# Kernel tuning notes

Hardware: AMD Instinct MI355X
Metric: run time of the kernel (lower is better)

The kernel has to match this reference:

```python
import jax, jax.numpy as jnp
import numpy as np

R = 256   # resolution
C = 16    # n_chan
F = 8     # n_freq
N = 262144


def setup_inputs() -> dict:
    key = jax.random.key(0)
    k1, k2 = jax.random.split(key)
    coords = jax.random.uniform(k1, (N, 3), dtype=jnp.float32, minval=-1.0, maxval=1.0)
    grid = jax.random.normal(k2, (3, C * F, R, R), dtype=jnp.float32) * 0.1
    # matches torch init: linspace(0,1,C*F).reshape(-1,C).T.reshape(-1)
    freqs = jnp.linspace(0.0, 1.0, C * F, dtype=jnp.float32).reshape(-1, C).T.reshape(-1)
    return {"coords": coords, "grid": grid, "freqs": freqs}


def _reflect(x, size):
    # PyTorch grid_sample reflection padding, align_corners=True:
    # reflect unnormalized coords about [0, size-1], period 2*(size-1)
    span = size - 1
    m = 2 * span
    r = jnp.abs(x) % m
    return jnp.where(r > span, m - r, r)


def _grid_sample_plane(img, xy):
    # img: (CF, R, R); xy: (Npts, 2) normalized [-1,1], (x indexes W, y indexes H)
    ix = _reflect((xy[:, 0] + 1.0) * 0.5 * (R - 1), R)
    iy = _reflect((xy[:, 1] + 1.0) * 0.5 * (R - 1), R)
    x0f = jnp.floor(ix); y0f = jnp.floor(iy)
    wx = ix - x0f; wy = iy - y0f
    x0 = jnp.clip(x0f.astype(jnp.int32), 0, R - 1)
    x1 = jnp.clip(x0 + 1, 0, R - 1)
    y0 = jnp.clip(y0f.astype(jnp.int32), 0, R - 1)
    y1 = jnp.clip(y0 + 1, 0, R - 1)
    v00 = img[:, y0, x0]  # (CF, Npts)
    v01 = img[:, y0, x1]
    v10 = img[:, y1, x0]
    v11 = img[:, y1, x1]
    return (v00 * (1 - wx) * (1 - wy) + v01 * wx * (1 - wy)
            + v10 * (1 - wx) * wy + v11 * wx * wy)


def reference(coords, grid, freqs):
    n = coords.shape[0]
    # tri-plane sample coords: plane0 (y,z), plane1 (x,z), plane2 (x,y)
    xy = jnp.stack([coords[:, (1, 2)], coords[:, (0, 2)], coords[:, (0, 1)]], 0)  # (3,N,2)
    coefs = jax.vmap(_grid_sample_plane)(grid, xy)          # (3, CF, N)
    coefs = coefs.transpose(2, 1, 0).reshape(n, C, F, 3)    # (N, C, F, 3)
    # get_freqs(): 2**(clamp(freqs,0,1)*log2(R)) - 1
    fr = 2.0 ** (jnp.clip(freqs, 0.0, 1.0) * np.float32(np.log2(R))) - 1.0  # (CF,)
    pts = (coords + 1.0) * 0.5 * (R - 1)                    # (N, 3)
    phase = (jnp.pi / R) * (pts[:, None, None, :] + 0.5) * (fr.reshape(C, F)[None, :, :, None] + 0.5)
    basis = jnp.cos(phase)                                   # (N, C, F, 3)
    # einsum BCFT,BCFT->BCT then sum over T == sum over (F, T)
    return 2.0 * jnp.sum(coefs * basis, axis=(2, 3))         # (N, C)
```

## Files before the change

### kernel.cpp

```cpp
#include <hip/hip_runtime.h>

#define RES   256
#define NCH   128
#define NC    16
#define QG    32
#define NPK   64
#define NBINS 4096

__device__ __forceinline__ unsigned int f32_to_bf16_rne(float f) {
    unsigned int u = __float_as_uint(f);
    return (u + 0x7FFFu + ((u >> 16) & 1u)) >> 16;
}
__device__ __forceinline__ float bf16_lo(unsigned int w) {
    return __uint_as_float(w << 16);
}
__device__ __forceinline__ float bf16_hi(unsigned int w) {
    return __uint_as_float(w & 0xFFFF0000u);
}
__device__ __forceinline__ float reflectf(float v) {
    float r = fabsf(v);
    r = fmodf(r, 510.0f);
    return (r > 255.0f) ? (510.0f - r) : r;
}
__device__ __forceinline__ unsigned spread3(unsigned v) {
    return (v & 1u) | ((v & 2u) << 2) | ((v & 4u) << 4) | ((v & 8u) << 6);
}
__device__ __forceinline__ int point_cell(const float* __restrict__ coords, int i) {
    const float r0 = reflectf((coords[3 * (size_t)i + 0] + 1.0f) * 127.5f);
    const float r1 = reflectf((coords[3 * (size_t)i + 1] + 1.0f) * 127.5f);
    const float r2 = reflectf((coords[3 * (size_t)i + 2] + 1.0f) * 127.5f);
    const unsigned cx = (unsigned)min(max((int)r0, 0), 255) >> 4;
    const unsigned cy = (unsigned)min(max((int)r1, 0), 255) >> 4;
    const unsigned cz = (unsigned)min(max((int)r2, 0), 255) >> 4;
    return (int)(spread3(cx) | (spread3(cy) << 1) | (spread3(cz) << 2));
}

__global__ __launch_bounds__(256) void fg_transpose_bf16(
    const float* __restrict__ in, unsigned int* __restrict__ out)
{
    __shared__ float tile[QG][RES + 4];
    const int tid = threadIdx.x;
    const int qg = blockIdx.x;
    const int y  = blockIdx.y;
    const int p  = blockIdx.z;
    const int q0 = qg * QG;

    const float* src = in + (((size_t)p * NCH + q0) * RES + y) * RES;
    #pragma unroll
    for (int it = 0; it < (QG * RES / 4) / 256; ++it) {
        const int lin = it * 256 + tid;
        const int qq = lin >> 6;
        const int x4 = lin & 63;
        *(float4*)&tile[qq][x4 * 4] =
            *(const float4*)(src + (size_t)qq * (RES * RES) + x4 * 4);
    }
    __syncthreads();
    unsigned int* dst = out + (((size_t)p * RES + y) * RES) * NPK + (q0 >> 1);
    #pragma unroll
    for (int it = 0; it < (RES * (QG / 2)) / 256; ++it) {
        const int lin = it * 256 + tid;
        const int qp = lin & 15;
        const int x  = lin >> 4;
        const unsigned int lo = f32_to_bf16_rne(tile[2 * qp + 0][x]);
        const unsigned int hi = f32_to_bf16_rne(tile[2 * qp + 1][x]);
        dst[(size_t)x * NPK + qp] = lo | (hi << 16);
    }
}

__global__ __launch_bounds__(256) void fg_hist(
    const float* __restrict__ coords, unsigned* __restrict__ hist, int n)
{
    const int i = blockIdx.x * 256 + threadIdx.x;
    if (i >= n) return;
    atomicAdd(&hist[point_cell(coords, i)], 1u);
}

__global__ __launch_bounds__(256) void fg_scan(
    const unsigned* __restrict__ hist, unsigned* __restrict__ cursor,
    const float* __restrict__ freqs, float* __restrict__ frp)
{
    __shared__ unsigned s[256];
    const int t = threadIdx.x;
    unsigned loc[16];
    unsigned sum = 0;
    #pragma unroll
    for (int k = 0; k < 16; ++k) { loc[k] = hist[t * 16 + k]; sum += loc[k]; }
    s[t] = sum;
    __syncthreads();
    for (int off = 1; off < 256; off <<= 1) {
        unsigned v = (t >= off) ? s[t - off] : 0u;
        __syncthreads();
        s[t] += v;
        __syncthreads();
    }
    unsigned base = (t == 0) ? 0u : s[t - 1];
    #pragma unroll
    for (int k = 0; k < 16; ++k) { cursor[t * 16 + k] = base; base += loc[k]; }
    if (t < 128) {
        const float f = fminf(fmaxf(freqs[t], 0.0f), 1.0f);
        frp[t] = __builtin_amdgcn_exp2f(f * 8.0f) - 0.5f;
    }
}

__global__ __launch_bounds__(256) void fg_scatter(
    const float* __restrict__ coords, unsigned* __restrict__ cursor,
    unsigned* __restrict__ perm, int n)
{
    const int i = blockIdx.x * 256 + threadIdx.x;
    if (i >= n) return;
    const unsigned pos = atomicAdd(&cursor[point_cell(coords, i)], 1u);
    perm[pos] = (unsigned)i;
}

__global__ __launch_bounds__(256) void fg_main_bf16(
    const float* __restrict__ coords,
    const unsigned int* __restrict__ grid,
    const float* __restrict__ frp_in,
    const unsigned* __restrict__ perm,
    float* __restrict__ out, int n)
{
    const int t = threadIdx.x;
    const int c = t & 15;
    const int slot = blockIdx.x * 16 + (t >> 4);
    if (slot >= n) return;
    const int i = (int)perm[slot];

    float frp[8];
    *(float4*)(frp + 0) = *(const float4*)(frp_in + c * 8 + 0);
    *(float4*)(frp + 4) = *(const float4*)(frp_in + c * 8 + 4);

    const float c0 = coords[3 * (size_t)i + 0];
    const float c1 = coords[3 * (size_t)i + 1];
    const float c2 = coords[3 * (size_t)i + 2];
    const float pts0 = (c0 + 1.0f) * 127.5f;
    const float pts1 = (c1 + 1.0f) * 127.5f;
    const float pts2 = (c2 + 1.0f) * 127.5f;

    float acc = 0.0f;

    #pragma unroll
    for (int p = 0; p < 3; ++p) {
        const float sx = (p == 0) ? pts1 : pts0;
        const float sy = (p == 2) ? pts1 : pts2;
        const float pp = (p == 0) ? pts0 : ((p == 1) ? pts1 : pts2);

        const float ix = reflectf(sx);
        const float iy = reflectf(sy);
        const float x0f = floorf(ix), y0f = floorf(iy);
        const float wx = ix - x0f, wy = iy - y0f;
        int x0 = (int)x0f; x0 = min(max(x0, 0), RES - 1);
        int y0 = (int)y0f; y0 = min(max(y0, 0), RES - 1);
        const int x1 = min(x0 + 1, RES - 1);
        const int y1 = min(y0 + 1, RES - 1);
        const float w00 = (1.0f - wx) * (1.0f - wy);
        const float w01 = wx * (1.0f - wy);
        const float w10 = (1.0f - wx) * wy;
        const float w11 = wx * wy;
        const float A = (pp + 0.5f) * (1.0f / 512.0f);

        const size_t rowbase = ((size_t)p * RES) * RES;
        const unsigned int* b00 = grid + (rowbase + (size_t)y0 * RES + x0) * NPK + c * 4;
        const unsigned int* b01 = grid + (rowbase + (size_t)y0 * RES + x1) * NPK + c * 4;
        const unsigned int* b10 = grid + (rowbase + (size_t)y1 * RES + x0) * NPK + c * 4;
        const unsigned int* b11 = grid + (rowbase + (size_t)y1 * RES + x1) * NPK + c * 4;
        const uint4 g00 = *(const uint4*)b00;
        const uint4 g01 = *(const uint4*)b01;
        const uint4 g10 = *(const uint4*)b10;
        const uint4 g11 = *(const uint4*)b11;
        const unsigned int w0[4] = {g00.x, g00.y, g00.z, g00.w};
        const unsigned int w1[4] = {g01.x, g01.y, g01.z, g01.w};
        const unsigned int w2[4] = {g10.x, g10.y, g10.z, g10.w};
        const unsigned int w3[4] = {g11.x, g11.y, g11.z, g11.w};

        #pragma unroll
        for (int jj = 0; jj < 4; ++jj) {
            const float clo = w00 * bf16_lo(w0[jj]) + w01 * bf16_lo(w1[jj])
                            + w10 * bf16_lo(w2[jj]) + w11 * bf16_lo(w3[jj]);
            const float chi = w00 * bf16_hi(w0[jj]) + w01 * bf16_hi(w1[jj])
                            + w10 * bf16_hi(w2[jj]) + w11 * bf16_hi(w3[jj]);
            const float rl = __builtin_amdgcn_fractf(A * frp[2 * jj + 0]);
            const float rh = __builtin_amdgcn_fractf(A * frp[2 * jj + 1]);
            acc += clo * __builtin_amdgcn_cosf(rl);
            acc += chi * __builtin_amdgcn_cosf(rh);
        }
    }

    out[(size_t)i * NC + c] = 2.0f * acc;
}

__global__ __launch_bounds__(256) void fg_main_f32(
    const float* __restrict__ coords,
    const float* __restrict__ grid,
    const float* __restrict__ freqs,
    float* __restrict__ out, int n)
{
    const int t = threadIdx.x;
    const int c = t & 15;
    const int i = blockIdx.x * 16 + (t >> 4);
    if (i >= n) return;

    float frp[8];
    #pragma unroll
    for (int j = 0; j < 8; ++j) {
        float f = fminf(fmaxf(freqs[c * 8 + j], 0.0f), 1.0f);
        frp[j] = __builtin_amdgcn_exp2f(f * 8.0f) - 0.5f;
    }
    const float c0 = coords[3 * (size_t)i + 0];
    const float c1 = coords[3 * (size_t)i + 1];
    const float c2 = coords[3 * (size_t)i + 2];
    const float pts0 = (c0 + 1.0f) * 127.5f;
    const float pts1 = (c1 + 1.0f) * 127.5f;
    const float pts2 = (c2 + 1.0f) * 127.5f;
    float acc = 0.0f;
    #pragma unroll
    for (int p = 0; p < 3; ++p) {
        const float sx = (p == 0) ? pts1 : pts0;
        const float sy = (p == 2) ? pts1 : pts2;
        const float pp = (p == 0) ? pts0 : ((p == 1) ? pts1 : pts2);
        const float ix = reflectf(sx);
        const float iy = reflectf(sy);
        const float x0f = floorf(ix), y0f = floorf(iy);
        const float wx = ix - x0f, wy = iy - y0f;
        int x0 = (int)x0f; x0 = min(max(x0, 0), RES - 1);
        int y0 = (int)y0f; y0 = min(max(y0, 0), RES - 1);
        const int x1 = min(x0 + 1, RES - 1);
        const int y1 = min(y0 + 1, RES - 1);
        const float w00 = (1.0f - wx) * (1.0f - wy);
        const float w01 = wx * (1.0f - wy);
        const float w10 = (1.0f - wx) * wy;
        const float w11 = wx * wy;
        const float A = (pp + 0.5f) * (1.0f / 512.0f);
        const size_t plane = (size_t)p * NCH * RES * RES;
        const int o00 = y0 * RES + x0, o01 = y0 * RES + x1;
        const int o10 = y1 * RES + x0, o11 = y1 * RES + x1;
        #pragma unroll
        for (int j = 0; j < 8; ++j) {
            const float* gq = grid + plane + (size_t)(c * 8 + j) * (RES * RES);
            const float coef = w00 * gq[o00] + w01 * gq[o01]
                             + w10 * gq[o10] + w11 * gq[o11];
            const float rr = __builtin_amdgcn_fractf(A * frp[j]);
            acc += coef * __builtin_amdgcn_cosf(rr);
        }
    }
    out[(size_t)i * NC + c] = 2.0f * acc;
}

extern "C" void kernel_launch(void* const* d_in, const int* in_sizes, int n_in,
                              void* d_out, int out_size, void* d_ws, size_t ws_size,
                              hipStream_t stream)
{
    const float* coords = (const float*)d_in[0];
    const float* grid   = (const float*)d_in[1];
    const float* freqs  = (const float*)d_in[2];
    float* out = (float*)d_out;
    const int n = in_sizes[0] / 3;

    const size_t gridT_b  = (size_t)3 * RES * RES * NPK * sizeof(unsigned);
    const size_t hist_b   = (size_t)NBINS * sizeof(unsigned);
    const size_t frp_b    = 128 * sizeof(float);
    const size_t perm_b   = (size_t)((n + 3) & ~3) * sizeof(unsigned);
    const size_t need = gridT_b + 2 * hist_b + frp_b + perm_b;

    const int blocks = (n + 15) / 16;

    if (ws_size >= need) {
        char* ws = (char*)d_ws;
        unsigned* gridT  = (unsigned*)ws;                 ws += gridT_b;
        unsigned* hist   = (unsigned*)ws;                 ws += hist_b;
        unsigned* cursor = (unsigned*)ws;                 ws += hist_b;
        float*    frp    = (float*)ws;                    ws += frp_b;
        unsigned* perm   = (unsigned*)ws;

        hipMemsetAsync(hist, 0, hist_b, stream);
        hipLaunchKernelGGL(fg_hist, dim3((n + 255) / 256), dim3(256), 0, stream,
                           coords, hist, n);
        hipLaunchKernelGGL(fg_scan, dim3(1), dim3(256), 0, stream,
                           hist, cursor, freqs, frp);
        hipLaunchKernelGGL(fg_scatter, dim3((n + 255) / 256), dim3(256), 0, stream,
                           coords, cursor, perm, n);
        hipLaunchKernelGGL(fg_transpose_bf16, dim3(4, RES, 3), dim3(256), 0, stream,
                           grid, gridT);
        hipLaunchKernelGGL(fg_main_bf16, dim3(blocks), dim3(256), 0, stream,
                           coords, gridT, frp, perm, out, n);
    } else {
        hipLaunchKernelGGL(fg_main_f32, dim3(blocks), dim3(256), 0, stream,
                           coords, grid, freqs, out, n);
    }
}
```

Measured before the change: 288.9 us.

## Fuse histogram into grid transpose, use wave-shuffle scan, and swizzle main block order

```diff
diff --git a/kernel.cpp b/kernel.cpp
--- a/kernel.cpp
+++ b/kernel.cpp
@@ -6,6 +6,7 @@
 #define QG    32
 #define NPK   64
 #define NBINS 4096
+#define TBLK  3072
 
 __device__ __forceinline__ unsigned int f32_to_bf16_rne(float f) {
     unsigned int u = __float_as_uint(f);
@@ -35,16 +36,26 @@
     return (int)(spread3(cx) | (spread3(cy) << 1) | (spread3(cz) << 2));
 }
 
-__global__ __launch_bounds__(256) void fg_transpose_bf16(
-    const float* __restrict__ in, unsigned int* __restrict__ out)
+__global__ __launch_bounds__(256) void fg_transpose_hist(
+    const float* __restrict__ in, unsigned int* __restrict__ out,
+    const float* __restrict__ coords, unsigned* __restrict__ hist, int n)
 {
     __shared__ float tile[QG][RES + 4];
     const int tid = threadIdx.x;
     const int qg = blockIdx.x;
     const int y  = blockIdx.y;
     const int p  = blockIdx.z;
+
+    {
+        const int bid = (p * RES + y) * 4 + qg;
+        const int per = (n + TBLK - 1) / TBLK;
+        const int s0 = bid * per;
+        const int s1 = min(s0 + per, n);
+        for (int k = s0 + tid; k < s1; k += 256)
+            atomicAdd(&hist[point_cell(coords, k)], 1u);
+    }
+
     const int q0 = qg * QG;
-
     const float* src = in + (((size_t)p * NCH + q0) * RES + y) * RES;
     #pragma unroll
     for (int it = 0; it < (QG * RES / 4) / 256; ++it) {
@@ -67,35 +78,32 @@
     }
 }
 
-__global__ __launch_bounds__(256) void fg_hist(
-    const float* __restrict__ coords, unsigned* __restrict__ hist, int n)
-{
-    const int i = blockIdx.x * 256 + threadIdx.x;
-    if (i >= n) return;
-    atomicAdd(&hist[point_cell(coords, i)], 1u);
-}
-
 __global__ __launch_bounds__(256) void fg_scan(
     const unsigned* __restrict__ hist, unsigned* __restrict__ cursor,
     const float* __restrict__ freqs, float* __restrict__ frp)
 {
-    __shared__ unsigned s[256];
+    __shared__ unsigned wtot[4];
     const int t = threadIdx.x;
+    const int lane = t & 63;
+    const int wid = t >> 6;
     unsigned loc[16];
     unsigned sum = 0;
     #pragma unroll
     for (int k = 0; k < 16; ++k) { loc[k] = hist[t * 16 + k]; sum += loc[k]; }
-    s[t] = sum;
+    unsigned v = sum;
+    #pragma unroll
+    for (int off = 1; off < 64; off <<= 1) {
+        unsigned u = __shfl_up(v, off);
+        if (lane >= off) v += u;
+    }
+    if (lane == 63) wtot[wid] = v;
     __syncthreads();
-    for (int off = 1; off < 256; off <<= 1) {
-        unsigned v = (t >= off) ? s[t - off] : 0u;
-        __syncthreads();
-        s[t] += v;
-        __syncthreads();
-    }
-    unsigned base = (t == 0) ? 0u : s[t - 1];
-    #pragma unroll
-    for (int k = 0; k < 16; ++k) { cursor[t * 16 + k] = base; base += loc[k]; }
+    unsigned base = 0;
+    #pragma unroll
+    for (int w = 0; w < 4; ++w) base += (w < wid) ? wtot[w] : 0u;
+    unsigned run = base + (v - sum);
+    #pragma unroll
+    for (int k = 0; k < 16; ++k) { cursor[t * 16 + k] = run; run += loc[k]; }
     if (t < 128) {
         const float f = fminf(fmaxf(freqs[t], 0.0f), 1.0f);
         frp[t] = __builtin_amdgcn_exp2f(f * 8.0f) - 0.5f;
@@ -121,7 +129,14 @@
 {
     const int t = threadIdx.x;
     const int c = t & 15;
-    const int slot = blockIdx.x * 16 + (t >> 4);
+    int b = blockIdx.x;
+    {
+        const int G = gridDim.x;
+        const int chunk = G >> 3;
+        const int lim = chunk << 3;
+        if (b < lim) b = (b & 7) * chunk + (b >> 3);
+    }
+    const int slot = b * 16 + (t >> 4);
     if (slot >= n) return;
     const int i = (int)perm[slot];
 
@@ -272,14 +287,12 @@
         unsigned* perm   = (unsigned*)ws;
 
         hipMemsetAsync(hist, 0, hist_b, stream);
-        hipLaunchKernelGGL(fg_hist, dim3((n + 255) / 256), dim3(256), 0, stream,
-                           coords, hist, n);
+        hipLaunchKernelGGL(fg_transpose_hist, dim3(4, RES, 3), dim3(256), 0, stream,
+                           grid, gridT, coords, hist, n);
         hipLaunchKernelGGL(fg_scan, dim3(1), dim3(256), 0, stream,
                            hist, cursor, freqs, frp);
         hipLaunchKernelGGL(fg_scatter, dim3((n + 255) / 256), dim3(256), 0, stream,
                            coords, cursor, perm, n);
-        hipLaunchKernelGGL(fg_transpose_bf16, dim3(4, RES, 3), dim3(256), 0, stream,
-                           grid, gridT);
         hipLaunchKernelGGL(fg_main_bf16, dim3(blocks), dim3(256), 0, stream,
                            coords, gridT, frp, perm, out, n);
     } else {
```

After: 244.3 us. 1.18x faster.
